# Kernel tuning notes

Hardware: AMD Instinct MI355X
Metric: run time of the kernel (lower is better)

The kernel has to match this reference:

```python
import jax, jax.numpy as jnp
import numpy as np

B, T, C, H = 2, 2048, 1024, 16
HS = C // H  # 64
EPS = 1e-5


def layernorm(x, g, b):
    mu = jnp.mean(x, axis=-1, keepdims=True)
    var = jnp.var(x, axis=-1, keepdims=True)
    return (x - mu) * jax.lax.rsqrt(var + EPS) * g + b


def setup_inputs() -> dict:
    key = jax.random.key(0)
    ks = jax.random.split(key, 12)
    s = lambda fan_in: 1.0 / np.sqrt(fan_in)
    inp = {
        'x':  jax.random.normal(ks[0], (B, T, C), dtype=jnp.float32),
        'Wq': jax.random.uniform(ks[1], (H, C, HS), jnp.float32, -s(C), s(C)),
        'Wk': jax.random.uniform(ks[2], (H, C, HS), jnp.float32, -s(C), s(C)),
        'Wv': jax.random.uniform(ks[3], (H, C, HS), jnp.float32, -s(C), s(C)),
        'Wp': jax.random.uniform(ks[4], (C, C), jnp.float32, -s(C), s(C)),
        'bp': jax.random.uniform(ks[5], (C,), jnp.float32, -s(C), s(C)),
        'W1': jax.random.uniform(ks[6], (C, 4 * C), jnp.float32, -s(C), s(C)),
        'b1': jax.random.uniform(ks[7], (4 * C,), jnp.float32, -s(C), s(C)),
        'W2': jax.random.uniform(ks[8], (4 * C, C), jnp.float32, -s(4 * C), s(4 * C)),
        'b2': jax.random.uniform(ks[9], (C,), jnp.float32, -s(4 * C), s(4 * C)),
        'g1': jnp.ones((C,), jnp.float32),
        'be1': jnp.zeros((C,), jnp.float32),
        'g2': jnp.ones((C,), jnp.float32),
        'be2': jnp.zeros((C,), jnp.float32),
    }
    return inp


def block(x, Wq, Wk, Wv, Wp, bp, W1, b1, W2, b2, g1, be1, g2, be2):
    # quirky residual structure: residual is taken from the post-LN tensor
    x = layernorm(x, g1, be1)
    # batched multi-head attention (all heads at once): [B,H,T,HS]
    q = jnp.einsum('btc,hcd->bhtd', x, Wq)
    k = jnp.einsum('btc,hcd->bhtd', x, Wk)
    v = jnp.einsum('btc,hcd->bhtd', x, Wv)
    # NOTE: original scales by full embedding dim C ** -0.5, not head_size
    scores = jnp.einsum('bhtd,bhsd->bhts', q, k) * (C ** -0.5)
    causal = jnp.tril(jnp.ones((T, T), dtype=bool))
    scores = jnp.where(causal, scores, -jnp.inf)
    wei = jax.nn.softmax(scores, axis=-1)  # dropout p=0 in eval
    out = jnp.einsum('bhts,bhsd->bhtd', wei, v)
    out = out.transpose(0, 2, 1, 3).reshape(B, T, C)  # concat heads
    out = out @ Wp + bp
    x = x + out
    x = layernorm(x, g2, be2)
    ff = jax.nn.relu(x @ W1 + b1) @ W2 + b2
    return x + ff


def reference(x, Wq, Wk, Wv, Wp, bp, W1, b1, W2, b2, g1, be1, g2, be2):
    return block(x, Wq, Wk, Wv, Wp, bp, W1, b1, W2, b2, g1, be1, g2, be2)
```

## Files before the change

kernel.cpp:

```cpp
#include <hip/hip_runtime.h>
#include <hip/hip_bf16.h>
#include <cstdint>
#include <cstddef>

typedef __attribute__((ext_vector_type(8))) short short8;
typedef __attribute__((ext_vector_type(4))) float f32x4;
typedef __attribute__((ext_vector_type(16))) float f32x16;
typedef unsigned int u32;
typedef unsigned short u16;

__device__ inline u16 f2b(float x) {
    union { float f; u32 u; } v; v.f = x;
    u32 u = v.u;
    u32 r = (u + 0x7fff + ((u >> 16) & 1)) >> 16;
    return (u16)r;
}
__device__ inline u32 cvtpk(float lo, float hi) {
    u32 r; asm("v_cvt_pk_bf16_f32 %0, %1, %2" : "=v"(r) : "v"(lo), "v"(hi)); return r;
}
__device__ inline void gll16(const void* g, void* l) {
    __builtin_amdgcn_global_load_lds(
        (const __attribute__((address_space(1))) void*)g,
        (__attribute__((address_space(3))) void*)l, 16, 0, 0);
}

__global__ __launch_bounds__(256) void repack_qkv_tiled(
    const float* __restrict__ Wq, const float* __restrict__ Wk, const float* __restrict__ Wv,
    u16* __restrict__ out)
{
    __shared__ u16 lds[64 * 72];
    const int tid = threadIdx.x;
    const int c0 = blockIdx.x * 64;
    const int sh = blockIdx.y;
    const int sel = sh >> 4, h = sh & 15;
    const float* W = (sel == 0) ? Wq : (sel == 1) ? Wk : Wv;
    #pragma unroll
    for (int it = 0; it < 4; ++it) {
        int idx = tid + it * 256;
        int c = idx >> 4, d4 = idx & 15;
        float4 v = *reinterpret_cast<const float4*>(&W[((size_t)(h * 1024 + c0 + c)) * 64 + d4 * 4]);
        lds[(d4 * 4 + 0) * 72 + c] = f2b(v.x);
        lds[(d4 * 4 + 1) * 72 + c] = f2b(v.y);
        lds[(d4 * 4 + 2) * 72 + c] = f2b(v.z);
        lds[(d4 * 4 + 3) * 72 + c] = f2b(v.w);
    }
    __syncthreads();
    #pragma unroll
    for (int it = 0; it < 2; ++it) {
        int idx = tid + it * 256;
        int d = idx >> 3, c8 = idx & 7;
        short8 s = *reinterpret_cast<const short8*>(&lds[d * 72 + c8 * 8]);
        *reinterpret_cast<short8*>(&out[((size_t)(sel * 1024 + h * 64 + d)) * 1024 + c0 + c8 * 8]) = s;
    }
}

__global__ __launch_bounds__(256) void trans_tiled(
    const float* __restrict__ in, u16* __restrict__ out, int P, int Q)
{
    __shared__ u16 lds[64 * 72];
    const int tid = threadIdx.x;
    const int p0 = blockIdx.x * 64, q0 = blockIdx.y * 64;
    #pragma unroll
    for (int it = 0; it < 4; ++it) {
        int idx = tid + it * 256;
        int p = idx >> 4, q4 = idx & 15;
        float4 v = *reinterpret_cast<const float4*>(&in[(size_t)(p0 + p) * Q + q0 + q4 * 4]);
        lds[(q4 * 4 + 0) * 72 + p] = f2b(v.x);
        lds[(q4 * 4 + 1) * 72 + p] = f2b(v.y);
        lds[(q4 * 4 + 2) * 72 + p] = f2b(v.z);
        lds[(q4 * 4 + 3) * 72 + p] = f2b(v.w);
    }
    __syncthreads();
    #pragma unroll
    for (int it = 0; it < 2; ++it) {
        int idx = tid + it * 256;
        int q = idx >> 3, p8 = idx & 7;
        short8 s = *reinterpret_cast<const short8*>(&lds[q * 72 + p8 * 8]);
        *reinterpret_cast<short8*>(&out[(size_t)(q0 + q) * P + p0 + p8 * 8]) = s;
    }
}

__global__ __launch_bounds__(256) void vt_kernel(
    const u16* __restrict__ qkv, u16* __restrict__ vt)
{
    __shared__ u16 lds[64 * 72];
    const int tid = threadIdx.x;
    const int s0 = blockIdx.x * 64, h = blockIdx.y, b = blockIdx.z;
    #pragma unroll
    for (int it = 0; it < 2; ++it) {
        int idx = tid + it * 256;
        int s = idx >> 3, d8 = idx & 7;
        short8 kv = *reinterpret_cast<const short8*>(
            &qkv[((size_t)(b * 2048 + s0 + s)) * 3072 + 2048 + h * 64 + d8 * 8]);
        #pragma unroll
        for (int j = 0; j < 8; ++j) lds[(d8 * 8 + j) * 72 + s] = (u16)kv[j];
    }
    __syncthreads();
    #pragma unroll
    for (int it = 0; it < 2; ++it) {
        int idx = tid + it * 256;
        int d = idx >> 3, s8 = idx & 7;
        short8 s = *reinterpret_cast<const short8*>(&lds[d * 72 + s8 * 8]);
        *reinterpret_cast<short8*>(&vt[((size_t)(b * 16 + h) * 64 + d) * 2048 + s0 + s8 * 8]) = s;
    }
}

__global__ __launch_bounds__(256) void ln_kernel(
    const float* __restrict__ x, const float* __restrict__ g, const float* __restrict__ be,
    float* __restrict__ yf, u16* __restrict__ yb)
{
    int row = blockIdx.x;
    const float4 v = reinterpret_cast<const float4*>(x + (size_t)row * 1024)[threadIdx.x];
    float s  = v.x + v.y + v.z + v.w;
    float s2 = v.x * v.x + v.y * v.y + v.z * v.z + v.w * v.w;
    #pragma unroll
    for (int o = 32; o >= 1; o >>= 1) { s += __shfl_xor(s, o); s2 += __shfl_xor(s2, o); }
    __shared__ float red[8];
    int w = threadIdx.x >> 6;
    if ((threadIdx.x & 63) == 0) { red[w] = s; red[4 + w] = s2; }
    __syncthreads();
    s  = red[0] + red[1] + red[2] + red[3];
    s2 = red[4] + red[5] + red[6] + red[7];
    float mu = s * (1.0f / 1024.0f);
    float var = s2 * (1.0f / 1024.0f) - mu * mu;
    float rs = rsqrtf(var + 1e-5f);
    const float4 gg = reinterpret_cast<const float4*>(g)[threadIdx.x];
    const float4 bb = reinterpret_cast<const float4*>(be)[threadIdx.x];
    float4 o;
    o.x = (v.x - mu) * rs * gg.x + bb.x;
    o.y = (v.y - mu) * rs * gg.y + bb.y;
    o.z = (v.z - mu) * rs * gg.z + bb.z;
    o.w = (v.w - mu) * rs * gg.w + bb.w;
    reinterpret_cast<float4*>(yf + (size_t)row * 1024)[threadIdx.x] = o;
    uint2 pk;
    pk.x = (u32)f2b(o.x) | ((u32)f2b(o.y) << 16);
    pk.y = (u32)f2b(o.z) | ((u32)f2b(o.w) << 16);
    reinterpret_cast<uint2*>(yb + (size_t)row * 1024)[threadIdx.x] = pk;
}

template<bool BIAS, bool RELU, bool RESID, bool OUTB>
__global__ __launch_bounds__(256) void gemm_bt(
    const u16* __restrict__ A, int lda,
    const u16* __restrict__ BT, int ldb,
    void* __restrict__ out, int ldo,
    const float* __restrict__ bias,
    const float* __restrict__ resid,
    int K)
{
    __shared__ __align__(16) char smem[64 * 1024];
    const int tid = threadIdx.x;
    const int lane = tid & 63, w = tid >> 6;
    const int wr = w >> 1, wc = w & 1;
    const int l15 = lane & 15, lq = lane >> 4;

    const int nx = gridDim.x;
    const int nwg = nx * gridDim.y;
    int orig = blockIdx.y * nx + blockIdx.x;
    int wgid = orig;
    if ((nwg & 7) == 0) wgid = (orig & 7) * (nwg >> 3) + (orig >> 3);
    const int m0 = (wgid / nx) * 128, n0 = (wgid % nx) * 128;

    auto stage = [&](int kt, int buf) {
        char* As = smem + buf * 32768;
        char* Bs = smem + buf * 32768 + 16384;
        #pragma unroll
        for (int it = 0; it < 4; ++it) {
            int slot = it * 256 + tid;
            int row = slot >> 3, c8 = (slot & 7) ^ (row & 7);
            gll16(A + (size_t)(m0 + row) * lda + kt + c8 * 8, As + (it * 256 + w * 64) * 16);
        }
        #pragma unroll
        for (int it = 0; it < 4; ++it) {
            int slot = it * 256 + tid;
            int row = slot >> 3, c8 = (slot & 7) ^ (row & 7);
            gll16(BT + (size_t)(n0 + row) * ldb + kt + c8 * 8, Bs + (it * 256 + w * 64) * 16);
        }
    };

    f32x4 acc[4][4] = {};
    const int nk = K >> 6;

    stage(0, 0);
    __syncthreads();

    for (int t = 0; t < nk; ++t) {
        const char* As = smem + (t & 1) * 32768;
        const char* Bs = smem + (t & 1) * 32768 + 16384;
        if (t + 1 < nk) stage((t + 1) << 6, (t + 1) & 1);
        #pragma unroll
        for (int kk = 0; kk < 2; ++kk) {
            const int sc = kk * 4 + lq;
            short8 a[4], b[4];
            #pragma unroll
            for (int mi = 0; mi < 4; ++mi) {
                int row = wr * 64 + mi * 16 + l15;
                a[mi] = *reinterpret_cast<const short8*>(As + row * 128 + ((sc ^ (row & 7)) << 4));
            }
            #pragma unroll
            for (int ni = 0; ni < 4; ++ni) {
                int row = wc * 64 + ni * 16 + l15;
                b[ni] = *reinterpret_cast<const short8*>(Bs + row * 128 + ((sc ^ (row & 7)) << 4));
            }
            #pragma unroll
            for (int mi = 0; mi < 4; ++mi)
                #pragma unroll
                for (int ni = 0; ni < 4; ++ni)
                    acc[mi][ni] = __builtin_amdgcn_mfma_f32_16x16x32_bf16(a[mi], b[ni], acc[mi][ni], 0, 0, 0);
        }
        __syncthreads();
    }

    #pragma unroll
    for (int mi = 0; mi < 4; ++mi) {
        #pragma unroll
        for (int ni = 0; ni < 4; ++ni) {
            int col = n0 + wc * 64 + ni * 16 + l15;
            float bv = BIAS ? bias[col] : 0.0f;
            #pragma unroll
            for (int r = 0; r < 4; ++r) {
                int row = m0 + wr * 64 + mi * 16 + lq * 4 + r;
                float v = acc[mi][ni][r] + bv;
                if (RELU) v = v > 0.0f ? v : 0.0f;
                if (RESID) v += resid[(size_t)row * ldo + col];
                if (OUTB) ((u16*)out)[(size_t)row * ldo + col] = f2b(v);
                else      ((float*)out)[(size_t)row * ldo + col] = v;
            }
        }
    }
}

__global__ __launch_bounds__(256, 2) void attn_kernel(
    const u16* __restrict__ qkv, const u16* __restrict__ vt, u16* __restrict__ att)
{
    __shared__ __align__(16) char smem[48 * 1024];
    char* Kb0 = smem;
    char* Kb1 = smem + 8192;
    char* Vb0 = smem + 16384;
    char* Vb1 = smem + 24576;
    char* Ost = smem + 32768;

    const int tid = threadIdx.x, lane = tid & 63, w = tid >> 6;
    const int l31 = lane & 31, hi = lane >> 5;
    const int bh = blockIdx.x;
    const int qbi = 15 - blockIdx.y;
    const int b = bh >> 4, h = bh & 15;
    const size_t base = (size_t)b * 2048;
    const int q0w = qbi * 128 + w * 32;
    const int nst = 2 * qbi + 2;
    const int kcol = 1024 + h * 64;
    const u16* vtp = vt + (size_t)bh * 64 * 2048;

    short8 qf[4];
    {
        const u16* qp = qkv + (base + q0w + l31) * 3072 + h * 64 + hi * 8;
        #pragma unroll
        for (int dc = 0; dc < 4; ++dc)
            qf[dc] = *reinterpret_cast<const short8*>(qp + dc * 16);
    }

    auto stage = [&](int st, char* kb, char* vb) {
        #pragma unroll
        for (int i = 0; i < 2; ++i) {
            int seg = w * 2 + i;
            int slot = seg * 64 + lane;
            int s = slot >> 3, d8p = slot & 7;
            gll16(qkv + (base + st * 64 + s) * 3072 + kcol + ((d8p ^ (s & 7)) * 8),
                  kb + seg * 1024);
            int d = s, s8p = d8p;
            gll16(vtp + (size_t)d * 2048 + st * 64 + ((s8p ^ (d & 7)) * 8),
                  vb + seg * 1024);
        }
    };

    f32x16 oT[2] = {};
    float m = -1e30f, lsum = 0.0f;
    const float scale = 0.03125f;
    const int qg = q0w + l31;

    stage(0, Kb0, Vb0);
    __syncthreads();

    for (int st = 0; st < nst; ++st) {
        char* kb = (st & 1) ? Kb1 : Kb0;
        char* vb = (st & 1) ? Vb1 : Vb0;
        if (st + 1 < nst) stage(st + 1, (st & 1) ? Kb0 : Kb1, (st & 1) ? Vb0 : Vb1);

        f32x16 sa[2] = {};
        #pragma unroll
        for (int dc = 0; dc < 4; ++dc) {
            #pragma unroll
            for (int sb = 0; sb < 2; ++sb) {
                int s = sb * 32 + l31;
                int slot = (dc * 2 + hi) ^ (s & 7);
                short8 kf = *reinterpret_cast<const short8*>(kb + s * 128 + slot * 16);
                sa[sb] = __builtin_amdgcn_mfma_f32_32x32x16_bf16(kf, qf[dc], sa[sb], 0, 0, 0);
            }
        }

        const bool maskt = (st >= nst - 2);
        float mx = -1e30f;
        #pragma unroll
        for (int sb = 0; sb < 2; ++sb)
            #pragma unroll
            for (int r = 0; r < 16; ++r) {
                float v = sa[sb][r] * scale;
                int sg = st * 64 + sb * 32 + (r & 3) + 8 * (r >> 2) + 4 * hi;
                if (maskt && sg > qg) v = -1e30f;
                sa[sb][r] = v;
                mx = fmaxf(mx, v);
            }
        mx = fmaxf(mx, __shfl_xor(mx, 32));
        float nm = fmaxf(m, mx);
        float sf = __expf(m - nm);
        m = nm;
        float ps = 0.0f;
        #pragma unroll
        for (int sb = 0; sb < 2; ++sb)
            #pragma unroll
            for (int r = 0; r < 16; ++r) {
                float p = __expf(sa[sb][r] - m);
                sa[sb][r] = p;
                ps += p;
            }
        ps += __shfl_xor(ps, 32);
        lsum = lsum * sf + ps;
        #pragma unroll
        for (int dt = 0; dt < 2; ++dt)
            #pragma unroll
            for (int r = 0; r < 16; ++r) oT[dt][r] *= sf;

        u32 pkE[4][2], pkO[4][2];
        #pragma unroll
        for (int sc = 0; sc < 4; ++sc) {
            const int sb = sc >> 1, rb = 8 * (sc & 1);
            #pragma unroll
            for (int c = 0; c < 2; ++c) {
                pkE[sc][c] = cvtpk(sa[sb][rb + 2 * c], sa[sb][rb + 2 * c + 1]);
                pkO[sc][c] = cvtpk(sa[sb][rb + 4 + 2 * c], sa[sb][rb + 4 + 2 * c + 1]);
            }
        }

        #pragma unroll
        for (int sc = 0; sc < 4; ++sc) {
            u32 wd[4];
            #pragma unroll
            for (int ww = 0; ww < 4; ++ww) {
                const int c = ww & 1;
                u32 own  = hi ? pkO[sc][c] : pkE[sc][c];
                u32 send = hi ? pkE[sc][c] : pkO[sc][c];
                u32 ex = (u32)__shfl_xor((int)send, 32);
                wd[ww] = ((ww >> 1) == hi) ? own : ex;
            }
            union { u32 u[4]; short8 s8; } pb_;
            pb_.u[0] = wd[0]; pb_.u[1] = wd[1]; pb_.u[2] = wd[2]; pb_.u[3] = wd[3];
            #pragma unroll
            for (int dt = 0; dt < 2; ++dt) {
                int d = dt * 32 + l31;
                int slot = (sc * 2 + hi) ^ (d & 7);
                short8 vf = *reinterpret_cast<const short8*>(vb + d * 128 + slot * 16);
                oT[dt] = __builtin_amdgcn_mfma_f32_32x32x16_bf16(vf, pb_.s8, oT[dt], 0, 0, 0);
            }
        }
        __syncthreads();
    }

    {
        float inv = 1.0f / lsum;
        char* ob = Ost + w * 4096;
        #pragma unroll
        for (int dt = 0; dt < 2; ++dt)
            #pragma unroll
            for (int rp = 0; rp < 8; ++rp) {
                int r = rp * 2;
                int d = dt * 32 + (r & 3) + 8 * (r >> 2) + 4 * hi;
                u32 pk2 = cvtpk(oT[dt][r] * inv, oT[dt][r + 1] * inv);
                int byte = l31 * 128 + ((((d >> 3) ^ (l31 & 7)) << 4)) + (d & 7) * 2;
                *reinterpret_cast<u32*>(ob + byte) = pk2;
            }
        __syncthreads();
        int q = lane >> 1, half = lane & 1;
        size_t grow = (base + q0w + q) * 1024 + h * 64 + half * 32;
        #pragma unroll
        for (int c = 0; c < 4; ++c) {
            int chunk = half * 4 + c;
            int byte = q * 128 + ((chunk ^ (q & 7)) << 4);
            float4 vv = *reinterpret_cast<const float4*>(ob + byte);
            *reinterpret_cast<float4*>(att + grow + c * 8) = vv;
        }
    }
}

extern "C" void kernel_launch(void* const* d_in, const int* in_sizes, int n_in,
                              void* d_out, int out_size, void* d_ws, size_t ws_size,
                              hipStream_t stream)
{
    const float* x   = (const float*)d_in[0];
    const float* Wq  = (const float*)d_in[1];
    const float* Wk  = (const float*)d_in[2];
    const float* Wv  = (const float*)d_in[3];
    const float* Wp  = (const float*)d_in[4];
    const float* bp  = (const float*)d_in[5];
    const float* W1  = (const float*)d_in[6];
    const float* b1  = (const float*)d_in[7];
    const float* W2  = (const float*)d_in[8];
    const float* b2  = (const float*)d_in[9];
    const float* g1  = (const float*)d_in[10];
    const float* be1 = (const float*)d_in[11];
    const float* g2  = (const float*)d_in[12];
    const float* be2 = (const float*)d_in[13];
    float* out = (float*)d_out;

    char* ws = (char*)d_ws;
    u16*   wqkvT = (u16*)(ws + 0);
    u16*   wpT   = (u16*)(ws + 6291456);
    u16*   w1T   = (u16*)(ws + 8388608);
    u16*   w2T   = (u16*)(ws + 16777216);
    float* xlnF  = (float*)(ws + 25165824);
    u16*   xlnB  = (u16*)(ws + 41943040);
    u16*   qkv   = (u16*)(ws + 50331648);
    float* x2    = (float*)(ws + 50331648);
    u16*   hbuf  = (u16*)(ws + 50331648);
    u16*   attb  = (u16*)(ws + 75497472);
    float* yF    = (float*)(ws + 83886080);
    u16*   vtb   = (u16*)(ws + 83886080);
    u16*   yB    = xlnB;

    repack_qkv_tiled<<<dim3(16, 48), 256, 0, stream>>>(Wq, Wk, Wv, wqkvT);
    trans_tiled<<<dim3(16, 16), 256, 0, stream>>>(Wp, wpT, 1024, 1024);
    trans_tiled<<<dim3(16, 64), 256, 0, stream>>>(W1, w1T, 1024, 4096);
    trans_tiled<<<dim3(64, 16), 256, 0, stream>>>(W2, w2T, 4096, 1024);

    ln_kernel<<<4096, 256, 0, stream>>>(x, g1, be1, xlnF, xlnB);

    gemm_bt<false, false, false, true><<<dim3(24, 32), 256, 0, stream>>>(
        xlnB, 1024, wqkvT, 1024, qkv, 3072, nullptr, nullptr, 1024);

    vt_kernel<<<dim3(32, 16, 2), 256, 0, stream>>>(qkv, vtb);
    attn_kernel<<<dim3(32, 16), 256, 0, stream>>>(qkv, vtb, attb);

    gemm_bt<true, false, true, false><<<dim3(8, 32), 256, 0, stream>>>(
        attb, 1024, wpT, 1024, x2, 1024, bp, xlnF, 1024);

    ln_kernel<<<4096, 256, 0, stream>>>(x2, g2, be2, yF, yB);

    gemm_bt<true, true, false, true><<<dim3(32, 32), 256, 0, stream>>>(
        yB, 1024, w1T, 1024, hbuf, 4096, b1, nullptr, 1024);

    gemm_bt<true, false, true, false><<<dim3(8, 32), 256, 0, stream>>>(
        hbuf, 4096, w2T, 4096, out, 1024, b2, yF, 4096);
}
```

Baseline: 243.6 us.

## Use explicit vmcnt waits, raw barriers, exp2 softmax and lazy rescaling

In the GEMM and attention kernels, __syncthreads is replaced by explicit s_waitcnt vmcnt(N) plus s_barrier and sched_barrier. Only the current stage's async LDS loads are awaited, so the next stage's prefetch stays in flight while compute runs. The attention softmax now folds log2(e) into the scale and uses exp2f. It skips the running-max rescale of the accumulator unless the new max exceeds the old one by more than 8 (lazy rescaling), and it raises wave priority around the MFMA blocks. Correctness depends on the hard-coded vmcnt counts matching the number of issued loads. The bounded exp overflow from lazy rescaling trades some precision headroom for fewer multiplies.

```diff
diff --git a/kernel.cpp b/kernel.cpp
--- a/kernel.cpp
+++ b/kernel.cpp
@@ -181,12 +181,22 @@
     const int nk = K >> 6;
 
     stage(0, 0);
-    __syncthreads();
+    asm volatile("s_waitcnt vmcnt(0)" ::: "memory");
+    __builtin_amdgcn_s_barrier();
+    __builtin_amdgcn_sched_barrier(0);
 
     for (int t = 0; t < nk; ++t) {
         const char* As = smem + (t & 1) * 32768;
         const char* Bs = smem + (t & 1) * 32768 + 16384;
-        if (t + 1 < nk) stage((t + 1) << 6, (t + 1) & 1);
+        if (t + 1 < nk) {
+            stage((t + 1) << 6, (t + 1) & 1);
+            asm volatile("s_waitcnt vmcnt(8)" ::: "memory");
+        } else {
+            asm volatile("s_waitcnt vmcnt(0)" ::: "memory");
+        }
+        __builtin_amdgcn_s_barrier();
+        __builtin_amdgcn_sched_barrier(0);
+
         #pragma unroll
         for (int kk = 0; kk < 2; ++kk) {
             const int sc = kk * 4 + lq;
@@ -207,7 +217,9 @@
                 for (int ni = 0; ni < 4; ++ni)
                     acc[mi][ni] = __builtin_amdgcn_mfma_f32_16x16x32_bf16(a[mi], b[ni], acc[mi][ni], 0, 0, 0);
         }
-        __syncthreads();
+
+        __builtin_amdgcn_s_barrier();
+        __builtin_amdgcn_sched_barrier(0);
     }
 
     #pragma unroll
@@ -274,18 +286,28 @@
 
     f32x16 oT[2] = {};
     float m = -1e30f, lsum = 0.0f;
-    const float scale = 0.03125f;
+    const float SC = 0.03125f * 1.44269504f;
     const int qg = q0w + l31;
 
     stage(0, Kb0, Vb0);
-    __syncthreads();
+    asm volatile("s_waitcnt vmcnt(0)" ::: "memory");
+    __builtin_amdgcn_s_barrier();
+    __builtin_amdgcn_sched_barrier(0);
 
     for (int st = 0; st < nst; ++st) {
         char* kb = (st & 1) ? Kb1 : Kb0;
         char* vb = (st & 1) ? Vb1 : Vb0;
-        if (st + 1 < nst) stage(st + 1, (st & 1) ? Kb0 : Kb1, (st & 1) ? Vb0 : Vb1);
+        if (st + 1 < nst) {
+            stage(st + 1, (st & 1) ? Kb0 : Kb1, (st & 1) ? Vb0 : Vb1);
+            asm volatile("s_waitcnt vmcnt(4)" ::: "memory");
+        } else {
+            asm volatile("s_waitcnt vmcnt(0)" ::: "memory");
+        }
+        __builtin_amdgcn_s_barrier();
+        __builtin_amdgcn_sched_barrier(0);
 
         f32x16 sa[2] = {};
+        __builtin_amdgcn_s_setprio(1);
         #pragma unroll
         for (int dc = 0; dc < 4; ++dc) {
             #pragma unroll
@@ -296,6 +318,7 @@
                 sa[sb] = __builtin_amdgcn_mfma_f32_32x32x16_bf16(kf, qf[dc], sa[sb], 0, 0, 0);
             }
         }
+        __builtin_amdgcn_s_setprio(0);
 
         const bool maskt = (st >= nst - 2);
         float mx = -1e30f;
@@ -303,31 +326,34 @@
         for (int sb = 0; sb < 2; ++sb)
             #pragma unroll
             for (int r = 0; r < 16; ++r) {
-                float v = sa[sb][r] * scale;
+                float v = sa[sb][r] * SC;
                 int sg = st * 64 + sb * 32 + (r & 3) + 8 * (r >> 2) + 4 * hi;
                 if (maskt && sg > qg) v = -1e30f;
                 sa[sb][r] = v;
                 mx = fmaxf(mx, v);
             }
         mx = fmaxf(mx, __shfl_xor(mx, 32));
-        float nm = fmaxf(m, mx);
-        float sf = __expf(m - nm);
-        m = nm;
+        if (!__all(mx <= m + 8.0f)) {
+            float nm = fmaxf(m, mx);
+            float sf = exp2f(m - nm);
+            m = nm;
+            lsum *= sf;
+            #pragma unroll
+            for (int dt = 0; dt < 2; ++dt)
+                #pragma unroll
+                for (int r = 0; r < 16; ++r) oT[dt][r] *= sf;
+        }
         float ps = 0.0f;
         #pragma unroll
         for (int sb = 0; sb < 2; ++sb)
             #pragma unroll
             for (int r = 0; r < 16; ++r) {
-                float p = __expf(sa[sb][r] - m);
+                float p = exp2f(sa[sb][r] - m);
                 sa[sb][r] = p;
                 ps += p;
             }
         ps += __shfl_xor(ps, 32);
-        lsum = lsum * sf + ps;
-        #pragma unroll
-        for (int dt = 0; dt < 2; ++dt)
-            #pragma unroll
-            for (int r = 0; r < 16; ++r) oT[dt][r] *= sf;
+        lsum += ps;
 
         u32 pkE[4][2], pkO[4][2];
         #pragma unroll
@@ -353,6 +379,7 @@
             }
             union { u32 u[4]; short8 s8; } pb_;
             pb_.u[0] = wd[0]; pb_.u[1] = wd[1]; pb_.u[2] = wd[2]; pb_.u[3] = wd[3];
+            __builtin_amdgcn_s_setprio(1);
             #pragma unroll
             for (int dt = 0; dt < 2; ++dt) {
                 int d = dt * 32 + l31;
@@ -360,8 +387,11 @@
                 short8 vf = *reinterpret_cast<const short8*>(vb + d * 128 + slot * 16);
                 oT[dt] = __builtin_amdgcn_mfma_f32_32x32x16_bf16(vf, pb_.s8, oT[dt], 0, 0, 0);
             }
-        }
-        __syncthreads();
+            __builtin_amdgcn_s_setprio(0);
+        }
+
+        __builtin_amdgcn_s_barrier();
+        __builtin_amdgcn_sched_barrier(0);
     }
 
     {
```

Measured after the change: 260.1 us. 6.8% more time.
